# Optimization experiments

Hardware: AMD Instinct MI355X
Metric: run time of the kernel (lower is better)

The kernel has to match this reference:

```python
import jax, jax.numpy as jnp
import numpy as np

B, S = 8192, 2048
EPS = 1e-8
DISCOUNT_FACTOR = 0.99
AVERAGE_LAMBDA = 0.9


def setup_inputs() -> dict:
    key = jax.random.key(0)
    k1, k2 = jax.random.split(key)
    values = jax.random.normal(k1, (B, S + 1, 1), dtype=jnp.float32)
    rewards = jax.random.normal(k2, (B, S, 1), dtype=jnp.float32)
    dones = jnp.zeros((B, S, 1), dtype=jnp.float32)
    # parameters initialized as in the module: atanh of target values
    raw_gamma = jnp.arctanh(jnp.full((1,), DISCOUNT_FACTOR, dtype=jnp.float32))
    raw_lambd = jnp.arctanh(jnp.full((S,), AVERAGE_LAMBDA, dtype=jnp.float32))
    return {"values": values, "rewards": rewards, "dones": dones,
            "raw_gamma": raw_gamma, "raw_lambd": raw_lambd}


def reference(values, rewards, dones, raw_gamma, raw_lambd):
    # gamma = tanh(raw_gamma).clamp_min(1e-8); lambda likewise (per timestep)
    gamma = jnp.maximum(jnp.tanh(raw_gamma), EPS)      # [1]
    lam = jnp.maximum(jnp.tanh(raw_lambd), EPS)        # [S]
    # time-major for scan: [S, B, 1]
    v_next = jnp.swapaxes(values[:, 1:], 0, 1)
    r = jnp.swapaxes(rewards, 0, 1)
    d = jnp.swapaxes(dones, 0, 1)

    def step(G, xs):
        vt1, rt, dt, lt = xs
        # G_t = r_t + gamma*(1-d_t)*((1-lam_t)*V_{t+1} + lam_t*G_{t+1})
        G = rt + gamma * (1.0 - dt) * ((1.0 - lt) * vt1 + lt * G)
        return G, G

    G_last = values[:, -1]  # bootstrap: [B, 1]
    _, Gs = jax.lax.scan(step, G_last, (v_next, r, d, lam), reverse=True)
    return jnp.swapaxes(Gs, 0, 1)  # [B, S, 1]
```

## Files before the change

kernel.cpp:

```cpp
#include <hip/hip_runtime.h>
#include <math.h>

#define EPS_F 1e-8f

typedef float vfloat4 __attribute__((ext_vector_type(4)));
typedef float uafloat4 __attribute__((ext_vector_type(4), aligned(4)));

__device__ __forceinline__ float bcast0(float x) {
    return __uint_as_float(__builtin_amdgcn_readfirstlane(__float_as_uint(x)));
}

__global__ __launch_bounds__(256) void glam_scan_kernel(
    const float* __restrict__ values,
    const float* __restrict__ rewards,
    const float* __restrict__ dones,
    const float* __restrict__ raw_gamma,
    const float* __restrict__ raw_lambd,
    float* __restrict__ out,
    int B)
{
    constexpr int S  = 2048;
    constexpr int NP = 8;

    __shared__ float lam_lds[S];

    const int tid  = threadIdx.x;
    const int wave = (blockIdx.x * blockDim.x + tid) >> 6;
    const int lane = tid & 63;

    #pragma unroll
    for (int k = 0; k < S / 256; ++k) {
        const int t = (k << 8) + tid;
        lam_lds[t] = fmaxf(tanhf(raw_lambd[t]), EPS_F);
    }
    __syncthreads();

    if (wave >= B) return;

    const float gamma = fmaxf(tanhf(raw_gamma[0]), EPS_F);

    const size_t vbase = (size_t)wave * (size_t)(S + 1);
    const size_t base  = (size_t)wave * (size_t)S;
    const int lo4 = 4 * lane;

    const float vS = values[vbase + S];

    float a[NP][4], bb[NP][4];
    #pragma unroll
    for (int p = 0; p < NP; ++p) {
        const int e0 = (p << 8) + lo4;

        const vfloat4  r4 = *reinterpret_cast<const vfloat4*>(rewards + base + e0);
        const vfloat4  d4 = *reinterpret_cast<const vfloat4*>(dones   + base + e0);
        const uafloat4 v4 = *reinterpret_cast<const uafloat4*>(values + vbase + e0 + 1);
        const vfloat4  l4 = *reinterpret_cast<const vfloat4*>(&lam_lds[e0]);

        const float rr[4] = { r4.x, r4.y, r4.z, r4.w };
        const float dd[4] = { d4.x, d4.y, d4.z, d4.w };
        const float vv[4] = { v4.x, v4.y, v4.z, v4.w };
        const float ll[4] = { l4.x, l4.y, l4.z, l4.w };

        #pragma unroll
        for (int j = 0; j < 4; ++j) {
            const float c = gamma * (1.0f - dd[j]);
            a[p][j]  = fmaf(c * (1.0f - ll[j]), vv[j], rr[j]);
            bb[p][j] = c * ll[j];
        }
    }

    float A1[NP], P1[NP];
    float pA[NP], pP[NP];
    #pragma unroll
    for (int p = 0; p < NP; ++p) {
        float A = 0.0f, P = 1.0f;
        #pragma unroll
        for (int j = 3; j >= 0; --j) {
            A = fmaf(bb[p][j], A, a[p][j]);
            P *= bb[p][j];
        }
        #pragma unroll
        for (int d = 1; d < 64; d <<= 1) {
            float A2 = __shfl_down(A, d);
            float P2 = __shfl_down(P, d);
            const bool valid = (lane + d) < 64;
            A2 = valid ? A2 : 0.0f;
            P2 = valid ? P2 : 1.0f;
            A = fmaf(P, A2, A);
            P *= P2;
        }
        pA[p] = bcast0(A);
        pP[p] = bcast0(P);
        const float Ad = __shfl_down(A, 1);
        const float Pd = __shfl_down(P, 1);
        A1[p] = (lane == 63) ? 0.0f : Ad;
        P1[p] = (lane == 63) ? 1.0f : Pd;
    }

    float Gb[NP + 1];
    Gb[NP] = vS;
    #pragma unroll
    for (int p = NP - 1; p >= 0; --p)
        Gb[p] = fmaf(pP[p], Gb[p + 1], pA[p]);

    #pragma unroll
    for (int p = 0; p < NP; ++p) {
        float G = fmaf(P1[p], Gb[p + 1], A1[p]);
        float o[4];
        #pragma unroll
        for (int j = 3; j >= 0; --j) {
            G = fmaf(bb[p][j], G, a[p][j]);
            o[j] = G;
        }
        vfloat4 o4;
        o4.x = o[0]; o4.y = o[1]; o4.z = o[2]; o4.w = o[3];
        __builtin_nontemporal_store(o4,
            reinterpret_cast<vfloat4*>(out + base + (p << 8) + lo4));
    }
}

__global__ void glam_naive_kernel(const float* __restrict__ values,
                                  const float* __restrict__ rewards,
                                  const float* __restrict__ dones,
                                  const float* __restrict__ raw_gamma,
                                  const float* __restrict__ raw_lambd,
                                  float* __restrict__ out, int B, int S) {
    int b = blockIdx.x * blockDim.x + threadIdx.x;
    if (b >= B) return;
    const float gamma = fmaxf(tanhf(raw_gamma[0]), EPS_F);
    const size_t vbase = (size_t)b * (size_t)(S + 1);
    const size_t base  = (size_t)b * (size_t)S;
    float G = values[vbase + S];
    for (int t = S - 1; t >= 0; --t) {
        const float lt = fmaxf(tanhf(raw_lambd[t]), EPS_F);
        const float c  = gamma * (1.0f - dones[base + t]);
        G = rewards[base + t] + c * ((1.0f - lt) * values[vbase + t + 1] + lt * G);
        out[base + t] = G;
    }
}

extern "C" void kernel_launch(void* const* d_in, const int* in_sizes, int n_in,
                              void* d_out, int out_size, void* d_ws, size_t ws_size,
                              hipStream_t stream) {
    const float* values    = (const float*)d_in[0];
    const float* rewards   = (const float*)d_in[1];
    const float* dones     = (const float*)d_in[2];
    const float* raw_gamma = (const float*)d_in[3];
    const float* raw_lambd = (const float*)d_in[4];
    float* out = (float*)d_out;

    const int S = in_sizes[4];
    const int B = in_sizes[1] / S;

    if (S != 2048) {
        glam_naive_kernel<<<(B + 255) / 256, 256, 0, stream>>>(
            values, rewards, dones, raw_gamma, raw_lambd, out, B, S);
        return;
    }

    const int total_threads = B * 64;
    const int blocks = (total_threads + 255) / 256;

    glam_scan_kernel<<<blocks, 256, 0, stream>>>(
        values, rewards, dones, raw_gamma, raw_lambd, out, B);
}
```

Baseline: 48.72 us.

## Split each row's scan across two waves with an LDS carry handoff

Each row is now handled by two waves that each cover half of the 2048 timesteps, with four chunks per wave instead of eight. The second-half wave computes its segment's carry and passes it to the first-half wave through LDS after a block barrier. This halves per-wave register use and serial work and doubles the wave count, which should raise occupancy and latency hiding. The cost is an extra __syncthreads, half as many rows per block, and a fallback to the naive kernel when B is odd.

```diff
diff --git a/kernel.cpp b/kernel.cpp
--- a/kernel.cpp
+++ b/kernel.cpp
@@ -19,14 +19,18 @@
     float* __restrict__ out,
     int B)
 {
-    constexpr int S  = 2048;
-    constexpr int NP = 8;
+    constexpr int S    = 2048;
+    constexpr int HALF = 1024;
+    constexpr int NP   = 4;
 
     __shared__ float lam_lds[S];
+    __shared__ float carry_lds[2];
 
     const int tid  = threadIdx.x;
-    const int wave = (blockIdx.x * blockDim.x + tid) >> 6;
+    const int wib  = tid >> 6;
     const int lane = tid & 63;
+    const int rib  = wib >> 1;
+    const int half = wib & 1;
 
     #pragma unroll
     for (int k = 0; k < S / 256; ++k) {
@@ -35,20 +39,22 @@
     }
     __syncthreads();
 
-    if (wave >= B) return;
+    const int row = blockIdx.x * 2 + rib;
 
     const float gamma = fmaxf(tanhf(raw_gamma[0]), EPS_F);
 
-    const size_t vbase = (size_t)wave * (size_t)(S + 1);
-    const size_t base  = (size_t)wave * (size_t)S;
+    const size_t vbase = (size_t)row * (size_t)(S + 1);
+    const size_t base  = (size_t)row * (size_t)S;
+    const int t00 = half * HALF;
     const int lo4 = 4 * lane;
 
-    const float vS = values[vbase + S];
+    float vS = 0.0f;
+    if (half == 1) vS = values[vbase + S];
 
     float a[NP][4], bb[NP][4];
     #pragma unroll
     for (int p = 0; p < NP; ++p) {
-        const int e0 = (p << 8) + lo4;
+        const int e0 = t00 + (p << 8) + lo4;
 
         const vfloat4  r4 = *reinterpret_cast<const vfloat4*>(rewards + base + e0);
         const vfloat4  d4 = *reinterpret_cast<const vfloat4*>(dones   + base + e0);
@@ -97,10 +103,21 @@
     }
 
     float Gb[NP + 1];
-    Gb[NP] = vS;
-    #pragma unroll
-    for (int p = NP - 1; p >= 0; --p)
-        Gb[p] = fmaf(pP[p], Gb[p + 1], pA[p]);
+
+    if (half == 1) {
+        Gb[NP] = vS;
+        #pragma unroll
+        for (int p = NP - 1; p >= 0; --p)
+            Gb[p] = fmaf(pP[p], Gb[p + 1], pA[p]);
+        if (lane == 0) carry_lds[rib] = Gb[0];
+        __syncthreads();
+    } else {
+        __syncthreads();
+        Gb[NP] = carry_lds[rib];
+        #pragma unroll
+        for (int p = NP - 1; p >= 0; --p)
+            Gb[p] = fmaf(pP[p], Gb[p + 1], pA[p]);
+    }
 
     #pragma unroll
     for (int p = 0; p < NP; ++p) {
@@ -114,7 +131,7 @@
         vfloat4 o4;
         o4.x = o[0]; o4.y = o[1]; o4.z = o[2]; o4.w = o[3];
         __builtin_nontemporal_store(o4,
-            reinterpret_cast<vfloat4*>(out + base + (p << 8) + lo4));
+            reinterpret_cast<vfloat4*>(out + base + t00 + (p << 8) + lo4));
     }
 }
 
@@ -151,15 +168,13 @@
     const int S = in_sizes[4];
     const int B = in_sizes[1] / S;
 
-    if (S != 2048) {
+    if (S != 2048 || (B & 1)) {
         glam_naive_kernel<<<(B + 255) / 256, 256, 0, stream>>>(
             values, rewards, dones, raw_gamma, raw_lambd, out, B, S);
         return;
     }
 
-    const int total_threads = B * 64;
-    const int blocks = (total_threads + 255) / 256;
-
+    const int blocks = B / 2;
     glam_scan_kernel<<<blocks, 256, 0, stream>>>(
         values, rewards, dones, raw_gamma, raw_lambd, out, B);
 }
```

Measured after the change: 46.68 us. 4.2% less time.
